# Optimization experiments

Measured on AMD Instinct MI355X. Metric: run time of the kernel, lower is better.

The kernel has to match this reference:

```python
import jax, jax.numpy as jnp
import numpy as np

B, P, L = 16, 32, 512
M = 32
L_EVAL = 2048


def setup_inputs() -> dict:
    key = jax.random.key(0)
    k1, k2, k3, k4, k5, k6 = jax.random.split(key, 6)
    # Sorted, positive event times per (B, P) path in [0, 1)
    event_times = jnp.sort(jax.random.uniform(k1, (B, P, L), dtype=jnp.float32), axis=-1)
    # Positive Hawkes parameters (as if post-Softplus)
    mu = jax.random.uniform(k2, (B, M, P, L), dtype=jnp.float32, minval=0.05, maxval=1.0)
    alpha = jax.random.uniform(k3, (B, M, P, L), dtype=jnp.float32, minval=0.05, maxval=2.0)
    beta = jax.random.uniform(k4, (B, M, P, L), dtype=jnp.float32, minval=0.1, maxval=5.0)
    # Positive per-batch normalisation constants
    norm_constants = jax.random.uniform(k5, (B,), dtype=jnp.float32, minval=0.5, maxval=1.5)
    # Query times on the ORIGINAL time axis (normalized_times=False path)
    query_times = jax.random.uniform(k6, (B, P, L_EVAL), dtype=jnp.float32, minval=0.0, maxval=1.5)
    return {
        "query_times": query_times,
        "event_times": event_times,
        "mu": mu,
        "alpha": alpha,
        "beta": beta,
        "norm_constants": norm_constants,
    }


def reference(query_times, event_times, mu, alpha, beta, norm_constants):
    # query_times: [B,P,Le]; event_times: [B,P,L]; mu/alpha/beta: [B,M,P,L]; norm_constants: [B]
    b, p, le = query_times.shape
    m = mu.shape[1]
    nc = norm_constants.reshape(b, 1, 1)
    q_norm = query_times / nc  # map to normalised axis (normalized_times=False)

    # searchsorted per (B,P) row: index of last event strictly before t
    ss = jax.vmap(jax.vmap(lambda a, v: jnp.searchsorted(a, v, side="left")))
    last_idx = ss(event_times, q_norm).astype(jnp.int32) - 1      # [B,P,Le]
    last_idx_cl = jnp.maximum(last_idx, 0)                         # clamp(min=0)

    # Gather parameters of the latest preceding event along L
    gidx = jnp.broadcast_to(last_idx_cl[:, None, :, :], (b, m, p, le))
    mu_last = jnp.take_along_axis(mu, gidx, axis=3)                # [B,M,P,Le]
    alpha_last = jnp.take_along_axis(alpha, gidx, axis=3)
    beta_last = jnp.take_along_axis(beta, gidx, axis=3)

    t_last = jnp.take_along_axis(event_times, last_idx_cl, axis=2)  # [B,P,Le]
    t_last = jnp.where(last_idx == -1, jnp.zeros_like(t_last), t_last)

    delta_t = (q_norm - t_last)[:, None, :, :]                      # [B,1,P,Le]
    intensity = mu_last + (alpha_last - mu_last) * jnp.exp(-beta_last * delta_t)
    # back to original scale
    intensity = intensity / norm_constants.reshape(b, 1, 1, 1)
    return intensity
```

## Files before the change

kernel.cpp:

```cpp
#include <hip/hip_runtime.h>

#define B_  16
#define P_  32
#define L_  512
#define M_  32
#define LE_ 2048

#define MSPLIT 8
#define MC     (M_ / MSPLIT)

__global__ __launch_bounds__(256) void hawkes_intensity_kernel(
    const float* __restrict__ q,
    const float* __restrict__ ev,
    const float* __restrict__ mu,
    const float* __restrict__ alpha,
    const float* __restrict__ beta,
    const float* __restrict__ nc,
    float* __restrict__ out)
{
    __shared__ float sev[L_];
    __shared__ float smu[MSPLIT][L_];
    __shared__ float sal[MSPLIT][L_];
    __shared__ float sbe[MSPLIT][L_];

    const int bid = blockIdx.x;
    const int mc  = bid & (MC - 1);
    const int row = bid >> 2;
    const int b   = row / P_;
    const int p   = row % P_;
    const int m0  = mc * MSPLIT;
    const int tid = threadIdx.x;

    const float* evrow = ev + (size_t)row * L_;
    sev[tid]       = evrow[tid];
    sev[tid + 256] = evrow[tid + 256];

    const size_t pbase   = (((size_t)b * M_ + m0) * P_ + p) * L_;
    const size_t mstride = (size_t)P_ * L_;
    #pragma unroll
    for (int i = 0; i < 4; ++i) {
        const int fidx = tid + 256 * i;
        const int ml   = fidx >> 7;
        const int l4   = (fidx & 127) << 2;
        const size_t g = pbase + (size_t)ml * mstride + l4;
        *(float4*)&smu[ml][l4] = *(const float4*)(mu    + g);
        *(float4*)&sal[ml][l4] = *(const float4*)(alpha + g);
        *(float4*)&sbe[ml][l4] = *(const float4*)(beta  + g);
    }
    __syncthreads();

    const float ncv    = nc[b];
    const float inv_nc = (float)(1.0 / (double)ncv);
    const float* qrow  = q + (size_t)row * LE_;

    #pragma unroll
    for (int pass = 0; pass < 2; ++pass) {
        const int le0 = 1024 * pass + 4 * tid;
        const float4 qv = *(const float4*)(qrow + le0);

        int   idx[4];
        float dt[4];
        #pragma unroll
        for (int i = 0; i < 4; ++i) {
            const float qn = ((const float*)&qv)[i] * inv_nc;
            int pos = 0;
            #pragma unroll
            for (int half = 256; half >= 1; half >>= 1) {
                const int cand = pos + half;
                pos = (sev[cand - 1] < qn) ? cand : pos;
            }
            pos += (sev[pos] < qn) ? 1 : 0;
            const int last = pos - 1;
            idx[i] = (last < 0) ? 0 : last;
            const float tl = (last < 0) ? 0.0f : sev[idx[i]];
            dt[i] = qn - tl;
        }

        const size_t obase = (((size_t)b * M_ + m0) * P_ + p) * LE_ + le0;
        #pragma unroll
        for (int m = 0; m < MSPLIT; ++m) {
            float4 o;
            #pragma unroll
            for (int i = 0; i < 4; ++i) {
                const float mul = smu[m][idx[i]];
                const float al  = sal[m][idx[i]];
                const float be  = sbe[m][idx[i]];
                ((float*)&o)[i] = (mul + (al - mul) * __expf(-be * dt[i])) * inv_nc;
            }
            *(float4*)(out + obase + (size_t)m * ((size_t)P_ * LE_)) = o;
        }
    }
}

extern "C" void kernel_launch(void* const* d_in, const int* in_sizes, int n_in,
                              void* d_out, int out_size, void* d_ws, size_t ws_size,
                              hipStream_t stream) {
    const float* q     = (const float*)d_in[0];
    const float* ev    = (const float*)d_in[1];
    const float* mu    = (const float*)d_in[2];
    const float* alpha = (const float*)d_in[3];
    const float* beta  = (const float*)d_in[4];
    const float* nc    = (const float*)d_in[5];
    float* out = (float*)d_out;

    dim3 grid(B_ * P_ * MC);
    dim3 block(256);
    hipLaunchKernelGGL(hawkes_intensity_kernel, grid, block, 0, stream,
                       q, ev, mu, alpha, beta, nc, out);
}
```

Baseline: 49.09 us.

## Use direct-to-LDS parameter loads and overlap binary search with them

Parameter tiles are now loaded with global_load_lds straight into shared memory, skipping the register round trip. The block grows to 512 threads so each thread handles one float4 of queries and the two-pass loop goes away. The binary search over event times now runs before the barrier that protects the parameter tiles, so it overlaps with those loads still in flight. The kernel is close to memory-bound, so the gain may be small, and the explicit waitcnt and barrier sequence adds ordering risk.

```diff
diff --git a/kernel.cpp b/kernel.cpp
--- a/kernel.cpp
+++ b/kernel.cpp
@@ -9,7 +9,14 @@
 #define MSPLIT 8
 #define MC     (M_ / MSPLIT)
 
-__global__ __launch_bounds__(256) void hawkes_intensity_kernel(
+
+__device__ __forceinline__ void gload_lds16(const float* g, float* l) {
+    __builtin_amdgcn_global_load_lds(
+        (const __attribute__((address_space(1))) void*)g,
+        (__attribute__((address_space(3))) void*)l, 16, 0, 0);
+}
+
+__global__ __launch_bounds__(512) void hawkes_intensity_kernel(
     const float* __restrict__ q,
     const float* __restrict__ ev,
     const float* __restrict__ mu,
@@ -32,63 +39,67 @@
     const int tid = threadIdx.x;
 
     const float* evrow = ev + (size_t)row * L_;
-    sev[tid]       = evrow[tid];
-    sev[tid + 256] = evrow[tid + 256];
+    const float e0 = (tid < L_) ? evrow[tid] : 0.0f;
+    const float4 qv = *(const float4*)(q + (size_t)row * LE_ + 4 * tid);
+
+    sev[tid] = e0;
 
     const size_t pbase   = (((size_t)b * M_ + m0) * P_ + p) * L_;
     const size_t mstride = (size_t)P_ * L_;
     #pragma unroll
-    for (int i = 0; i < 4; ++i) {
-        const int fidx = tid + 256 * i;
+    for (int i = 0; i < 2; ++i) {
+        const int fidx = tid + 512 * i;
         const int ml   = fidx >> 7;
         const int l4   = (fidx & 127) << 2;
+        const int fb   = (tid & ~63) + 512 * i;
+        const int l4b  = (fb & 127) << 2;
         const size_t g = pbase + (size_t)ml * mstride + l4;
-        *(float4*)&smu[ml][l4] = *(const float4*)(mu    + g);
-        *(float4*)&sal[ml][l4] = *(const float4*)(alpha + g);
-        *(float4*)&sbe[ml][l4] = *(const float4*)(beta  + g);
+        gload_lds16(mu    + g, &smu[ml][l4b]);
+        gload_lds16(alpha + g, &sal[ml][l4b]);
+        gload_lds16(beta  + g, &sbe[ml][l4b]);
     }
-    __syncthreads();
+
+    asm volatile("s_waitcnt lgkmcnt(0)" ::: "memory");
+    __builtin_amdgcn_s_barrier();
+    __builtin_amdgcn_sched_barrier(0);
 
     const float ncv    = nc[b];
     const float inv_nc = (float)(1.0 / (double)ncv);
-    const float* qrow  = q + (size_t)row * LE_;
 
+    int   idx[4];
+    float dt[4];
     #pragma unroll
-    for (int pass = 0; pass < 2; ++pass) {
-        const int le0 = 1024 * pass + 4 * tid;
-        const float4 qv = *(const float4*)(qrow + le0);
+    for (int i = 0; i < 4; ++i) {
+        const float qn = ((const float*)&qv)[i] * inv_nc;
+        int pos = 0;
+        #pragma unroll
+        for (int half = 256; half >= 1; half >>= 1) {
+            const int cand = pos + half;
+            pos = (sev[cand - 1] < qn) ? cand : pos;
+        }
+        pos += (sev[pos] < qn) ? 1 : 0;
+        const int last = pos - 1;
+        idx[i] = (last < 0) ? 0 : last;
+        const float tl = (last < 0) ? 0.0f : sev[idx[i]];
+        dt[i] = qn - tl;
+    }
 
-        int   idx[4];
-        float dt[4];
+    __syncthreads();
+
+    const int le0 = 4 * tid;
+    const size_t obase = (((size_t)b * M_ + m0) * P_ + p) * LE_ + le0;
+    #pragma unroll
+    for (int m = 0; m < MSPLIT; ++m) {
+        float4 o;
         #pragma unroll
         for (int i = 0; i < 4; ++i) {
-            const float qn = ((const float*)&qv)[i] * inv_nc;
-            int pos = 0;
-            #pragma unroll
-            for (int half = 256; half >= 1; half >>= 1) {
-                const int cand = pos + half;
-                pos = (sev[cand - 1] < qn) ? cand : pos;
-            }
-            pos += (sev[pos] < qn) ? 1 : 0;
-            const int last = pos - 1;
-            idx[i] = (last < 0) ? 0 : last;
-            const float tl = (last < 0) ? 0.0f : sev[idx[i]];
-            dt[i] = qn - tl;
+            const int   ix  = idx[i];
+            const float mul = smu[m][ix];
+            const float al  = sal[m][ix];
+            const float be  = sbe[m][ix];
+            ((float*)&o)[i] = (mul + (al - mul) * __expf(-be * dt[i])) * inv_nc;
         }
-
-        const size_t obase = (((size_t)b * M_ + m0) * P_ + p) * LE_ + le0;
-        #pragma unroll
-        for (int m = 0; m < MSPLIT; ++m) {
-            float4 o;
-            #pragma unroll
-            for (int i = 0; i < 4; ++i) {
-                const float mul = smu[m][idx[i]];
-                const float al  = sal[m][idx[i]];
-                const float be  = sbe[m][idx[i]];
-                ((float*)&o)[i] = (mul + (al - mul) * __expf(-be * dt[i])) * inv_nc;
-            }
-            *(float4*)(out + obase + (size_t)m * ((size_t)P_ * LE_)) = o;
-        }
+        *(float4*)(out + obase + (size_t)m * ((size_t)P_ * LE_)) = o;
     }
 }
 
@@ -104,7 +115,7 @@
     float* out = (float*)d_out;
 
     dim3 grid(B_ * P_ * MC);
-    dim3 block(256);
+    dim3 block(512);
     hipLaunchKernelGGL(hawkes_intensity_kernel, grid, block, 0, stream,
                        q, ev, mu, alpha, beta, nc, out);
 }
```

Result: faster. 43.36 us (-11.7%).
